# Kernel tuning notes

Measured on AMD Instinct MI355X. Metric: run time of the kernel, lower is better.

Reference implementation:

```python
import jax, jax.numpy as jnp
import numpy as np

B, T, C, S, H, K = 32, 128, 32, 256, 64, 3  # T == 2*H required by final Linear(hidden*2, 1)


def setup_inputs() -> dict:
    key = jax.random.key(0)
    k1, k2, k3, k4 = jax.random.split(key, 4)
    x = jax.random.normal(k1, (B, T, C, S), jnp.float32)
    # ConvLSTMCell: Conv1d(C+H -> 4H, kernel K, padding same), gate order i,f,o,g
    Wc = jax.random.normal(k2, (4 * H, C + H, K), jnp.float32) * 0.05
    bc = jnp.zeros((4 * H,), jnp.float32)
    # final Linear(hidden*2 = T, 1)
    Wl = jax.random.normal(k3, (1, T), jnp.float32) * 0.05
    bl = jnp.zeros((1,), jnp.float32)
    return {"x": x, "Wc": Wc, "bc": bc, "Wl": Wl, "bl": bl}


def _cell(x_t, h, c, Wc, bc):
    # x_t: (B, C, T); h, c: (B, H, T). Conv over the T axis, 'same' padding.
    z = jnp.concatenate([x_t, h], axis=1)  # (B, C+H, T)
    conv = jax.lax.conv_general_dilated(
        z, Wc, window_strides=(1,), padding='SAME',
        dimension_numbers=('NCH', 'OIH', 'NCH')) + bc[None, :, None]
    ci, cf, co, cg = jnp.split(conv, 4, axis=1)
    i = jax.nn.sigmoid(ci)
    f = jax.nn.sigmoid(cf)
    o = jax.nn.sigmoid(co)
    g = jnp.tanh(cg)
    c_next = f * c + i * g
    h_next = o * jnp.tanh(c_next)
    return h_next, c_next


def reference(x, Wc, bc, Wl, bl):
    # x: (B, T, C, S); sequential scan over spatial axis S with (h, c) recurrence.
    xs = jnp.transpose(x, (3, 0, 2, 1))  # (S, B, C, T)
    h0 = jnp.zeros((x.shape[0], H, x.shape[1]), x.dtype)

    def step(carry, xt):
        h, c = carry
        h2, c2 = _cell(xt, h, c, Wc, bc)
        return (h2, c2), h2

    _, hs = jax.lax.scan(step, (h0, h0), xs)  # hs: (S, B, H, T)
    lstm_out = jnp.transpose(hs, (1, 0, 2, 3))  # (B, S, H, T)
    out = jax.nn.sigmoid(jnp.einsum('bsht,ot->bso', lstm_out, Wl)[..., None].squeeze(-1)[..., None] * 0 + jnp.einsum('bsht,ot->bsho', lstm_out, Wl) + bl)
    return out  # (B, S, H, 1)
```

## Files before the change

kernel.cpp:

```cpp
#include <hip/hip_runtime.h>


#define Bb 32
#define Tt 128
#define Cc 32
#define Ss 256
#define Hh 64
#define ZST 104

typedef __bf16 bf16x8 __attribute__((ext_vector_type(8)));
typedef short  short8 __attribute__((ext_vector_type(8)));
typedef float  f32x4  __attribute__((ext_vector_type(4)));
typedef unsigned short u16;
typedef unsigned int   u32;

__device__ __forceinline__ u16 f2bf(float f) {
    u32 u = __float_as_uint(f);
    u = (u + 0x7FFFu + ((u >> 16) & 1u)) >> 16;
    return (u16)u;
}
__device__ __forceinline__ float fsig(float x) {
    float e = __expf(-x);
    return __builtin_amdgcn_rcpf(1.0f + e);
}
__device__ __forceinline__ float ftanh_(float x) {
    float e = __expf(2.0f * x);
    return 1.0f - 2.0f * __builtin_amdgcn_rcpf(e + 1.0f);
}

__global__ __launch_bounds__(256) void xpose_kernel(const float* __restrict__ x,
                                                    u16* __restrict__ xT) {
    __shared__ u16 tile[64][130];
    const int tc0 = blockIdx.x * 128;
    const int s0  = blockIdx.y * 64;
    const int b   = blockIdx.z;
    const int tid = threadIdx.x;
    const float* xb = x + (size_t)b * (Tt * Cc * Ss);
#pragma unroll
    for (int i = 0; i < 32; ++i) {
        const int tcr = (tid >> 6) + 4 * i;
        const int sr  = tid & 63;
        tile[sr][tcr] = f2bf(xb[(size_t)(tc0 + tcr) * Ss + s0 + sr]);
    }
    __syncthreads();
    u32* xTo = (u32*)(xT + (size_t)b * (Ss * Tt * Cc));
#pragma unroll
    for (int j = 0; j < 16; ++j) {
        const int sw = (tid >> 6) + 4 * j;
        const int tw = (tid & 63) * 2;
        xTo[(((size_t)(s0 + sw)) * (Tt * Cc) + tc0 + tw) >> 1] = *(const u32*)&tile[sw][tw];
    }
}

__global__ __launch_bounds__(256) void wprep_kernel(const float* __restrict__ Wc,
                                                    u16* __restrict__ wpre) {
    const int ht  = blockIdx.x;
    const int tid = threadIdx.x;
#pragma unroll
    for (int it = 0; it < 9; ++it) {
        const int idx  = it * 256 + tid;
        const int f    = idx >> 6;
        const int lane = idx & 63;
        const int g  = f / 9;
        const int k  = (f % 9) / 3;
        const int ks = f % 3;
        const int l15 = lane & 15;
        const int q   = lane >> 4;
        const int gc  = 64 * g + 16 * ht + l15;
        u16 tmp[8];
#pragma unroll
        for (int j = 0; j < 8; ++j)
            tmp[j] = f2bf(Wc[gc * 288 + (32 * ks + 8 * q + j) * 3 + k]);
        *(uint4*)(wpre + ((size_t)(ht * 36 + f) * 64 + lane) * 8) = *(const uint4*)tmp;
    }
}

__global__ __launch_bounds__(512) void convlstm5_kernel(
    const float* __restrict__ bc, const float* __restrict__ Wl,
    const float* __restrict__ bl, const u16* __restrict__ xT,
    const u16* __restrict__ wpre, float* __restrict__ out) {

    __shared__ u16  zbuf[2][130][ZST];
    __shared__ float red[8][16];

    const int b    = blockIdx.x;
    const int tid  = threadIdx.x;
    const int w    = tid >> 6;
    const int lane = tid & 63;
    const int l15  = lane & 15;
    const int q    = lane >> 4;
    const int ht   = w >> 1;
    const int th   = w & 1;

    {
        u32* z32 = (u32*)&zbuf[0][0][0];
        for (int i = tid; i < (2 * 130 * ZST) / 2; i += 512) z32[i] = 0;
    }

    const u16* wlp = wpre + (size_t)ht * 18432 + lane * 8;

    f32x4 bcv[4];
#pragma unroll
    for (int g = 0; g < 4; ++g) bcv[g] = *(const f32x4*)&bc[64 * g + 16 * ht + 4 * q];
    float wlv[4];
#pragma unroll
    for (int nj = 0; nj < 4; ++nj) wlv[nj] = Wl[64 * th + 16 * nj + l15];
    const float bl0 = bl[0];

    float cst[16];
#pragma unroll
    for (int i = 0; i < 16; ++i) cst[i] = 0.0f;

    const int xt = tid >> 2;
    const int xc = (tid & 3) * 8;
    const u16* xTb = xT + (size_t)b * (Ss * Tt * Cc);

    {
        uint4 xv0 = *(const uint4*)(xTb + xt * 32 + xc);
        __syncthreads();
        *(uint4*)&zbuf[0][1 + xt][xc] = xv0;
        __syncthreads();
    }

    float* outb = out + (size_t)b * (Ss * Hh);
    int p = 0;

    for (int s = 0; s < Ss; ++s) {
        uint4 xv;
        const bool havex = (s + 1) < Ss;
        if (havex) xv = *(const uint4*)(xTb + (size_t)(s + 1) * (Tt * Cc) + xt * 32 + xc);

        if (tid < 64 && s > 0) {
            float v = red[(tid >> 4) * 2][tid & 15] + red[(tid >> 4) * 2 + 1][tid & 15] + bl0;
            outb[(size_t)(s - 1) * Hh + tid] = fsig(v);
        }
        __syncthreads();

        const u16 (*zb)[ZST] = zbuf[p];
        u16 (*zn)[ZST] = zbuf[p ^ 1];

        float partial[4] = {0.f, 0.f, 0.f, 0.f};

#pragma unroll
        for (int half = 0; half < 2; ++half) {
            f32x4 acc[4][2];
#pragma unroll
            for (int g = 0; g < 4; ++g) {
                acc[g][0] = bcv[g];
                acc[g][1] = bcv[g];
            }

            bf16x8 wf[2][4];
#pragma unroll
            for (int g = 0; g < 4; ++g)
                wf[0][g] = *(const bf16x8*)(wlp + (size_t)(g * 9) * 512);

#pragma unroll
            for (int kk = 0; kk < 9; ++kk) {
                const int k  = kk / 3;
                const int ks = kk % 3;
                const int cur = kk & 1;
                if (kk < 8) {
#pragma unroll
                    for (int g = 0; g < 4; ++g)
                        wf[cur ^ 1][g] = *(const bf16x8*)(wlp + (size_t)(g * 9 + kk + 1) * 512);
                }
#pragma unroll
                for (int njl = 0; njl < 2; ++njl) {
                    const int nj = half * 2 + njl;
                    const int tb = 64 * th + 16 * nj + l15;
                    bf16x8 bfr = *(const bf16x8*)&zb[tb + k][32 * ks + 8 * q];
                    acc[0][njl] = __builtin_amdgcn_mfma_f32_16x16x32_bf16(wf[cur][0], bfr, acc[0][njl], 0, 0, 0);
                    acc[1][njl] = __builtin_amdgcn_mfma_f32_16x16x32_bf16(wf[cur][1], bfr, acc[1][njl], 0, 0, 0);
                    acc[2][njl] = __builtin_amdgcn_mfma_f32_16x16x32_bf16(wf[cur][2], bfr, acc[2][njl], 0, 0, 0);
                    acc[3][njl] = __builtin_amdgcn_mfma_f32_16x16x32_bf16(wf[cur][3], bfr, acc[3][njl], 0, 0, 0);
                }
            }

#pragma unroll
            for (int njl = 0; njl < 2; ++njl) {
                const int nj = half * 2 + njl;
                u16 hp[4];
#pragma unroll
                for (int r = 0; r < 4; ++r) {
                    const float ig = fsig(acc[0][njl][r]);
                    const float fg = fsig(acc[1][njl][r]);
                    const float og = fsig(acc[2][njl][r]);
                    const float gg = ftanh_(acc[3][njl][r]);
                    const float cv = fg * cst[nj * 4 + r] + ig * gg;
                    cst[nj * 4 + r] = cv;
                    const float hv = og * ftanh_(cv);
                    partial[r] += hv * wlv[nj];
                    hp[r] = f2bf(hv);
                }
                uint2 hw;
                hw.x = (u32)hp[0] | ((u32)hp[1] << 16);
                hw.y = (u32)hp[2] | ((u32)hp[3] << 16);
                *(uint2*)&zn[1 + 64 * th + 16 * nj + l15][32 + 16 * ht + 4 * q] = hw;
            }
        }

        if (havex) *(uint4*)&zn[1 + xt][xc] = xv;

#pragma unroll
        for (int r = 0; r < 4; ++r) {
#pragma unroll
            for (int offl = 1; offl <= 8; offl <<= 1)
                partial[r] += __shfl_xor(partial[r], offl, 64);
        }
        if (l15 == 0) {
#pragma unroll
            for (int r = 0; r < 4; ++r) red[w][4 * q + r] = partial[r];
        }
        __syncthreads();
        p ^= 1;
    }

    if (tid < 64) {
        float v = red[(tid >> 4) * 2][tid & 15] + red[(tid >> 4) * 2 + 1][tid & 15] + bl0;
        outb[(size_t)(Ss - 1) * Hh + tid] = fsig(v);
    }
}

__global__ __launch_bounds__(512, 2) void convlstm_kernel(
    const float* __restrict__ Wc, const float* __restrict__ bc,
    const float* __restrict__ Wl, const float* __restrict__ bl,
    const u16* __restrict__ xT, float* __restrict__ out) {

    __shared__ u16  zbuf[2][130][ZST];
    __shared__ float red[8][16];
    __shared__ float bcl[256];

    const int b    = blockIdx.x;
    const int tid  = threadIdx.x;
    const int w    = tid >> 6;
    const int lane = tid & 63;
    const int l15  = lane & 15;
    const int q    = lane >> 4;
    const int ht   = w >> 1;
    const int th   = w & 1;

    {
        u32* z32 = (u32*)&zbuf[0][0][0];
        for (int i = tid; i < (2 * 130 * ZST) / 2; i += 512) z32[i] = 0;
    }
    if (tid < 256) bcl[tid] = bc[tid];

    bf16x8 afr[4][3][3];
#pragma unroll
    for (int g = 0; g < 4; ++g)
#pragma unroll
        for (int k = 0; k < 3; ++k)
#pragma unroll
            for (int ks = 0; ks < 3; ++ks) {
                const int gc = 64 * g + 16 * ht + l15;
                short8 t;
#pragma unroll
                for (int j = 0; j < 8; ++j)
                    t[j] = (short)f2bf(Wc[gc * 288 + (32 * ks + 8 * q + j) * 3 + k]);
                afr[g][k][ks] = __builtin_bit_cast(bf16x8, t);
            }

    float wlv[4];
#pragma unroll
    for (int nj = 0; nj < 4; ++nj) wlv[nj] = Wl[64 * th + 16 * nj + l15];
    const float bl0 = bl[0];

    float cst[16];
#pragma unroll
    for (int i = 0; i < 16; ++i) cst[i] = 0.0f;

    const int xt = tid >> 2;
    const int xc = (tid & 3) * 8;
    const u16* xTb = xT + (size_t)b * (Ss * Tt * Cc);

    {
        uint4 xv0 = *(const uint4*)(xTb + xt * 32 + xc);
        __syncthreads();
        *(uint4*)&zbuf[0][1 + xt][xc] = xv0;
        __syncthreads();
    }

    float* outb = out + (size_t)b * (Ss * Hh);
    int p = 0;

    for (int s = 0; s < Ss; ++s) {
        uint4 xv;
        const bool havex = (s + 1) < Ss;
        if (havex) xv = *(const uint4*)(xTb + (size_t)(s + 1) * (Tt * Cc) + xt * 32 + xc);

        if (tid < 64 && s > 0) {
            float v = red[(tid >> 4) * 2][tid & 15] + red[(tid >> 4) * 2 + 1][tid & 15] + bl0;
            outb[(size_t)(s - 1) * Hh + tid] = fsig(v);
        }
        __syncthreads();

        const u16 (*zb)[ZST] = zbuf[p];
        u16 (*zn)[ZST] = zbuf[p ^ 1];

        float partial[4] = {0.f, 0.f, 0.f, 0.f};

#pragma unroll
        for (int half = 0; half < 2; ++half) {
            f32x4 acc[4][2];
#pragma unroll
            for (int g = 0; g < 4; ++g) {
                acc[g][0] = (f32x4){0.f, 0.f, 0.f, 0.f};
                acc[g][1] = (f32x4){0.f, 0.f, 0.f, 0.f};
            }
#pragma unroll
            for (int njl = 0; njl < 2; ++njl) {
                const int nj = half * 2 + njl;
                const int tb = 64 * th + 16 * nj + l15;
#pragma unroll
                for (int k = 0; k < 3; ++k)
#pragma unroll
                    for (int ks = 0; ks < 3; ++ks) {
                        bf16x8 bfr = *(const bf16x8*)&zb[tb + k][32 * ks + 8 * q];
                        acc[0][njl] = __builtin_amdgcn_mfma_f32_16x16x32_bf16(afr[0][k][ks], bfr, acc[0][njl], 0, 0, 0);
                        acc[1][njl] = __builtin_amdgcn_mfma_f32_16x16x32_bf16(afr[1][k][ks], bfr, acc[1][njl], 0, 0, 0);
                        acc[2][njl] = __builtin_amdgcn_mfma_f32_16x16x32_bf16(afr[2][k][ks], bfr, acc[2][njl], 0, 0, 0);
                        acc[3][njl] = __builtin_amdgcn_mfma_f32_16x16x32_bf16(afr[3][k][ks], bfr, acc[3][njl], 0, 0, 0);
                    }
            }

#pragma unroll
            for (int njl = 0; njl < 2; ++njl) {
                const int nj = half * 2 + njl;
                u16 hp[4];
#pragma unroll
                for (int r = 0; r < 4; ++r) {
                    const int hl = 4 * q + r;
                    const float ig = fsig(acc[0][njl][r] + bcl[0   + 16 * ht + hl]);
                    const float fg = fsig(acc[1][njl][r] + bcl[64  + 16 * ht + hl]);
                    const float og = fsig(acc[2][njl][r] + bcl[128 + 16 * ht + hl]);
                    const float gg = ftanh_(acc[3][njl][r] + bcl[192 + 16 * ht + hl]);
                    const float cv = fg * cst[nj * 4 + r] + ig * gg;
                    cst[nj * 4 + r] = cv;
                    const float hv = og * ftanh_(cv);
                    partial[r] += hv * wlv[nj];
                    hp[r] = f2bf(hv);
                }
                uint2 hw;
                hw.x = (u32)hp[0] | ((u32)hp[1] << 16);
                hw.y = (u32)hp[2] | ((u32)hp[3] << 16);
                *(uint2*)&zn[1 + 64 * th + 16 * nj + l15][32 + 16 * ht + 4 * q] = hw;
            }
        }

        if (havex) *(uint4*)&zn[1 + xt][xc] = xv;

#pragma unroll
        for (int r = 0; r < 4; ++r) {
#pragma unroll
            for (int offl = 1; offl <= 8; offl <<= 1)
                partial[r] += __shfl_xor(partial[r], offl, 64);
        }
        if (l15 == 0) {
#pragma unroll
            for (int r = 0; r < 4; ++r) red[w][4 * q + r] = partial[r];
        }
        __syncthreads();
        p ^= 1;
    }

    if (tid < 64) {
        float v = red[(tid >> 4) * 2][tid & 15] + red[(tid >> 4) * 2 + 1][tid & 15] + bl0;
        outb[(size_t)(Ss - 1) * Hh + tid] = fsig(v);
    }
}

extern "C" void kernel_launch(void* const* d_in, const int* in_sizes, int n_in,
                              void* d_out, int out_size, void* d_ws, size_t ws_size,
                              hipStream_t stream) {
    const float* x  = (const float*)d_in[0];
    const float* Wc = (const float*)d_in[1];
    const float* bc = (const float*)d_in[2];
    const float* Wl = (const float*)d_in[3];
    const float* bl = (const float*)d_in[4];
    float* out = (float*)d_out;

    u16* xT = (u16*)d_ws;
    const size_t XT_BYTES = (size_t)Bb * Ss * Tt * Cc * 2;
    const size_t WP_BYTES = (size_t)4 * 36 * 64 * 8 * 2;

    dim3 tgrid(Tt * Cc / 128, Ss / 64, Bb);
    xpose_kernel<<<tgrid, 256, 0, stream>>>(x, xT);

    if (ws_size >= XT_BYTES + WP_BYTES) {
        u16* wpre = (u16*)((char*)d_ws + XT_BYTES);
        wprep_kernel<<<4, 256, 0, stream>>>(Wc, wpre);
        convlstm5_kernel<<<Bb, 512, 0, stream>>>(bc, Wl, bl, xT, wpre, out);
    } else {
        convlstm_kernel<<<Bb, 512, 0, stream>>>(Wc, bc, Wl, bl, xT, out);
    }
}
```

Measured before the change: 1.375 ms.

## Split each batch recurrence across two workgroups with global-memory halo exchange

Replaces the one-block-per-batch recurrent kernel with two cooperating workgroups per batch, each computing half of the hidden channels. The blocks exchange their new h slices every step through a global halo buffer guarded by release/acquire flag counters. Each block also caches its half of the prepacked weights in LDS and uses a hardware packed bf16 conversion. This doubles the number of CUs working on the sequential scan (64 blocks instead of 32) and halves per-step MFMA work per block. The cost is a global-memory spin-wait every step, and forward progress relies on both blocks of a pair being resident at the same time.

```diff
diff --git a/kernel.cpp b/kernel.cpp
--- a/kernel.cpp
+++ b/kernel.cpp
@@ -13,6 +13,7 @@
 typedef float  f32x4  __attribute__((ext_vector_type(4)));
 typedef unsigned short u16;
 typedef unsigned int   u32;
+typedef unsigned long long u64;
 
 __device__ __forceinline__ u16 f2bf(float f) {
     u32 u = __float_as_uint(f);
@@ -26,6 +27,11 @@
 __device__ __forceinline__ float ftanh_(float x) {
     float e = __expf(2.0f * x);
     return 1.0f - 2.0f * __builtin_amdgcn_rcpf(e + 1.0f);
+}
+__device__ __forceinline__ u32 cvtpk(float lo, float hi) {
+    u32 d;
+    asm("v_cvt_pk_bf16_f32 %0, %1, %2" : "=v"(d) : "v"(lo), "v"(hi));
+    return d;
 }
 
 __global__ __launch_bounds__(256) void xpose_kernel(const float* __restrict__ x,
@@ -75,13 +81,182 @@
     }
 }
 
-__global__ __launch_bounds__(512) void convlstm5_kernel(
+__global__ __launch_bounds__(512) void convlstm6_kernel(
     const float* __restrict__ bc, const float* __restrict__ Wl,
     const float* __restrict__ bl, const u16* __restrict__ xT,
-    const u16* __restrict__ wpre, float* __restrict__ out) {
-
+    const u16* __restrict__ wpre, u64* __restrict__ halo,
+    u32* __restrict__ flags, float* __restrict__ out) {
+
+    __shared__ u16  wlds[36864];
     __shared__ u16  zbuf[2][130][ZST];
     __shared__ float red[8][16];
+
+    const int p    = blockIdx.x;
+    const int b    = blockIdx.y;
+    const int tid  = threadIdx.x;
+    const int w    = tid >> 6;
+    const int lane = tid & 63;
+    const int l15  = lane & 15;
+    const int q    = lane >> 4;
+    const int th   = w >> 1;
+    const int ht2  = w & 1;
+
+    {
+        u32* z32 = (u32*)&zbuf[0][0][0];
+        for (int i = tid; i < (2 * 130 * ZST) / 2; i += 512) z32[i] = 0;
+    }
+    {
+        const uint4* wsrc = (const uint4*)(wpre + (size_t)(2 * p) * 18432);
+        uint4* wdst = (uint4*)wlds;
+#pragma unroll
+        for (int i = 0; i < 9; ++i) wdst[tid + 512 * i] = wsrc[tid + 512 * i];
+    }
+
+    f32x4 bcv[4];
+#pragma unroll
+    for (int g = 0; g < 4; ++g)
+        bcv[g] = *(const f32x4*)&bc[64 * g + 32 * p + 16 * ht2 + 4 * q];
+    float wlv[2];
+#pragma unroll
+    for (int nj = 0; nj < 2; ++nj) wlv[nj] = Wl[32 * th + 16 * nj + l15];
+    const float bl0 = bl[0];
+
+    float cst[8];
+#pragma unroll
+    for (int i = 0; i < 8; ++i) cst[i] = 0.0f;
+
+    const int xr = tid >> 2;
+    const int xc = (tid & 3) * 8;
+    const u16* xTb = xT + (size_t)b * (Ss * Tt * Cc);
+
+    u64* haloP = halo + (size_t)(b * 2 + p) * 2 * 1024;
+    const u64* haloC = halo + (size_t)(b * 2 + (1 - p)) * 2 * 1024;
+    u32* flagP = flags + (b * 2 + p) * 2;
+    u32* flagC = flags + (b * 2 + (1 - p)) * 2;
+
+    {
+        uint4 xv0 = *(const uint4*)(xTb + xr * 32 + xc);
+        __syncthreads();
+        *(uint4*)&zbuf[1][1 + xr][xc] = xv0;
+        __syncthreads();
+    }
+
+    float* outb = out + (size_t)b * (Ss * Hh) + 32 * p;
+    const u16* wl0 = wlds + ht2 * 18432 + lane * 8;
+
+    for (int s = 0; s < Ss; ++s) {
+        uint4 xv;
+        const bool havex = (s + 1) < Ss;
+        if (havex) xv = *(const uint4*)(xTb + (size_t)(s + 1) * (Tt * Cc) + xr * 32 + xc);
+
+        if (tid < 32 && s > 0) {
+            const int h2 = tid >> 4, hh = tid & 15;
+            float v = red[h2][hh] + red[2 + h2][hh] + red[4 + h2][hh] + red[6 + h2][hh] + bl0;
+            outb[(size_t)(s - 1) * Hh + 16 * h2 + hh] = fsig(v);
+        }
+        __syncthreads();
+
+        const u16 (*zb)[ZST] = zbuf[(s + 1) & 1];
+        u16 (*zn)[ZST] = zbuf[s & 1];
+
+        f32x4 acc[2][4];
+#pragma unroll
+        for (int nj = 0; nj < 2; ++nj)
+#pragma unroll
+            for (int g = 0; g < 4; ++g) acc[nj][g] = bcv[g];
+
+#pragma unroll
+        for (int k = 0; k < 3; ++k)
+#pragma unroll
+            for (int ks = 0; ks < 3; ++ks) {
+                bf16x8 wf0 = *(const bf16x8*)(wl0 + (0 * 9 + k * 3 + ks) * 512);
+                bf16x8 wf1 = *(const bf16x8*)(wl0 + (1 * 9 + k * 3 + ks) * 512);
+                bf16x8 wf2 = *(const bf16x8*)(wl0 + (2 * 9 + k * 3 + ks) * 512);
+                bf16x8 wf3 = *(const bf16x8*)(wl0 + (3 * 9 + k * 3 + ks) * 512);
+#pragma unroll
+                for (int nj = 0; nj < 2; ++nj) {
+                    bf16x8 bfr = *(const bf16x8*)&zb[32 * th + 16 * nj + l15 + k][32 * ks + 8 * q];
+                    acc[nj][0] = __builtin_amdgcn_mfma_f32_16x16x32_bf16(wf0, bfr, acc[nj][0], 0, 0, 0);
+                    acc[nj][1] = __builtin_amdgcn_mfma_f32_16x16x32_bf16(wf1, bfr, acc[nj][1], 0, 0, 0);
+                    acc[nj][2] = __builtin_amdgcn_mfma_f32_16x16x32_bf16(wf2, bfr, acc[nj][2], 0, 0, 0);
+                    acc[nj][3] = __builtin_amdgcn_mfma_f32_16x16x32_bf16(wf3, bfr, acc[nj][3], 0, 0, 0);
+                }
+            }
+
+        float partial[4] = {0.f, 0.f, 0.f, 0.f};
+#pragma unroll
+        for (int nj = 0; nj < 2; ++nj) {
+            float hv[4];
+#pragma unroll
+            for (int r = 0; r < 4; ++r) {
+                const float ig = fsig(acc[nj][0][r]);
+                const float fg = fsig(acc[nj][1][r]);
+                const float og = fsig(acc[nj][2][r]);
+                const float gg = ftanh_(acc[nj][3][r]);
+                const float cv = fg * cst[nj * 4 + r] + ig * gg;
+                cst[nj * 4 + r] = cv;
+                hv[r] = og * ftanh_(cv);
+                partial[r] += hv[r] * wlv[nj];
+            }
+            const u32 hx = cvtpk(hv[0], hv[1]);
+            const u32 hy = cvtpk(hv[2], hv[3]);
+            const int t = 32 * th + 16 * nj + l15;
+            uint2 hw; hw.x = hx; hw.y = hy;
+            *(uint2*)&zn[1 + t][32 + 32 * p + 16 * ht2 + 4 * q] = hw;
+            const u64 pv = (u64)hx | ((u64)hy << 32);
+            __hip_atomic_store(&haloP[(size_t)(s & 1) * 1024 + t * 8 + 4 * ht2 + q], pv,
+                               __ATOMIC_RELAXED, __HIP_MEMORY_SCOPE_AGENT);
+        }
+        if (lane == 0)
+            __hip_atomic_fetch_add(&flagP[s & 1], 1u, __ATOMIC_RELEASE, __HIP_MEMORY_SCOPE_AGENT);
+
+        if (havex) *(uint4*)&zn[1 + xr][xc] = xv;
+
+#pragma unroll
+        for (int r = 0; r < 4; ++r) {
+#pragma unroll
+            for (int offl = 1; offl <= 8; offl <<= 1)
+                partial[r] += __shfl_xor(partial[r], offl, 64);
+        }
+        if (l15 == 0) {
+#pragma unroll
+            for (int r = 0; r < 4; ++r) red[w][4 * q + r] = partial[r];
+        }
+
+        if (s + 1 < Ss) {
+            if (lane == 0) {
+                const u32 tgt = 8u * ((u32)(s >> 1) + 1u);
+                while (__hip_atomic_load(&flagC[s & 1], __ATOMIC_ACQUIRE,
+                                         __HIP_MEMORY_SCOPE_AGENT) < tgt) {}
+            }
+            const u64* hsrc = haloC + (size_t)(s & 1) * 1024;
+#pragma unroll
+            for (int ii = 0; ii < 2; ++ii) {
+                const int j = tid + 512 * ii;
+                const u64 v = __hip_atomic_load(&hsrc[j], __ATOMIC_RELAXED,
+                                                __HIP_MEMORY_SCOPE_AGENT);
+                uint2 vw; vw.x = (u32)v; vw.y = (u32)(v >> 32);
+                *(uint2*)&zn[1 + (j >> 3)][32 + 32 * (1 - p) + 4 * (j & 7)] = vw;
+            }
+        }
+        __syncthreads();
+    }
+
+    if (tid < 32) {
+        const int h2 = tid >> 4, hh = tid & 15;
+        float v = red[h2][hh] + red[2 + h2][hh] + red[4 + h2][hh] + red[6 + h2][hh] + bl0;
+        outb[(size_t)(Ss - 1) * Hh + 16 * h2 + hh] = fsig(v);
+    }
+}
+
+__global__ __launch_bounds__(512, 2) void convlstm_kernel(
+    const float* __restrict__ Wc, const float* __restrict__ bc,
+    const float* __restrict__ Wl, const float* __restrict__ bl,
+    const u16* __restrict__ xT, float* __restrict__ out) {
+
+    __shared__ u16  zbuf[2][130][ZST];
+    __shared__ float red[8][16];
+    __shared__ float bcl[256];
 
     const int b    = blockIdx.x;
     const int tid  = threadIdx.x;
@@ -96,12 +271,23 @@
         u32* z32 = (u32*)&zbuf[0][0][0];
         for (int i = tid; i < (2 * 130 * ZST) / 2; i += 512) z32[i] = 0;
     }
-
-    const u16* wlp = wpre + (size_t)ht * 18432 + lane * 8;
-
-    f32x4 bcv[4];
-#pragma unroll
-    for (int g = 0; g < 4; ++g) bcv[g] = *(const f32x4*)&bc[64 * g + 16 * ht + 4 * q];
+    if (tid < 256) bcl[tid] = bc[tid];
+
+    bf16x8 afr[4][3][3];
+#pragma unroll
+    for (int g = 0; g < 4; ++g)
+#pragma unroll
+        for (int k = 0; k < 3; ++k)
+#pragma unroll
+            for (int ks = 0; ks < 3; ++ks) {
+                const int gc = 64 * g + 16 * ht + l15;
+                short8 t;
+#pragma unroll
+                for (int j = 0; j < 8; ++j)
+                    t[j] = (short)f2bf(Wc[gc * 288 + (32 * ks + 8 * q + j) * 3 + k]);
+                afr[g][k][ks] = __builtin_bit_cast(bf16x8, t);
+            }
+
     float wlv[4];
 #pragma unroll
     for (int nj = 0; nj < 4; ++nj) wlv[nj] = Wl[64 * th + 16 * nj + l15];
@@ -123,7 +309,7 @@
     }
 
     float* outb = out + (size_t)b * (Ss * Hh);
-    int p = 0;
+    int pp = 0;
 
     for (int s = 0; s < Ss; ++s) {
         uint4 xv;
@@ -136,167 +322,8 @@
         }
         __syncthreads();
 
-        const u16 (*zb)[ZST] = zbuf[p];
-        u16 (*zn)[ZST] = zbuf[p ^ 1];
-
-        float partial[4] = {0.f, 0.f, 0.f, 0.f};
-
-#pragma unroll
-        for (int half = 0; half < 2; ++half) {
-            f32x4 acc[4][2];
-#pragma unroll
-            for (int g = 0; g < 4; ++g) {
-                acc[g][0] = bcv[g];
-                acc[g][1] = bcv[g];
-            }
-
-            bf16x8 wf[2][4];
-#pragma unroll
-            for (int g = 0; g < 4; ++g)
-                wf[0][g] = *(const bf16x8*)(wlp + (size_t)(g * 9) * 512);
-
-#pragma unroll
-            for (int kk = 0; kk < 9; ++kk) {
-                const int k  = kk / 3;
-                const int ks = kk % 3;
-                const int cur = kk & 1;
-                if (kk < 8) {
-#pragma unroll
-                    for (int g = 0; g < 4; ++g)
-                        wf[cur ^ 1][g] = *(const bf16x8*)(wlp + (size_t)(g * 9 + kk + 1) * 512);
-                }
-#pragma unroll
-                for (int njl = 0; njl < 2; ++njl) {
-                    const int nj = half * 2 + njl;
-                    const int tb = 64 * th + 16 * nj + l15;
-                    bf16x8 bfr = *(const bf16x8*)&zb[tb + k][32 * ks + 8 * q];
-                    acc[0][njl] = __builtin_amdgcn_mfma_f32_16x16x32_bf16(wf[cur][0], bfr, acc[0][njl], 0, 0, 0);
-                    acc[1][njl] = __builtin_amdgcn_mfma_f32_16x16x32_bf16(wf[cur][1], bfr, acc[1][njl], 0, 0, 0);
-                    acc[2][njl] = __builtin_amdgcn_mfma_f32_16x16x32_bf16(wf[cur][2], bfr, acc[2][njl], 0, 0, 0);
-                    acc[3][njl] = __builtin_amdgcn_mfma_f32_16x16x32_bf16(wf[cur][3], bfr, acc[3][njl], 0, 0, 0);
-                }
-            }
-
-#pragma unroll
-            for (int njl = 0; njl < 2; ++njl) {
-                const int nj = half * 2 + njl;
-                u16 hp[4];
-#pragma unroll
-                for (int r = 0; r < 4; ++r) {
-                    const float ig = fsig(acc[0][njl][r]);
-                    const float fg = fsig(acc[1][njl][r]);
-                    const float og = fsig(acc[2][njl][r]);
-                    const float gg = ftanh_(acc[3][njl][r]);
-                    const float cv = fg * cst[nj * 4 + r] + ig * gg;
-                    cst[nj * 4 + r] = cv;
-                    const float hv = og * ftanh_(cv);
-                    partial[r] += hv * wlv[nj];
-                    hp[r] = f2bf(hv);
-                }
-                uint2 hw;
-                hw.x = (u32)hp[0] | ((u32)hp[1] << 16);
-                hw.y = (u32)hp[2] | ((u32)hp[3] << 16);
-                *(uint2*)&zn[1 + 64 * th + 16 * nj + l15][32 + 16 * ht + 4 * q] = hw;
-            }
-        }
-
-        if (havex) *(uint4*)&zn[1 + xt][xc] = xv;
-
-#pragma unroll
-        for (int r = 0; r < 4; ++r) {
-#pragma unroll
-            for (int offl = 1; offl <= 8; offl <<= 1)
-                partial[r] += __shfl_xor(partial[r], offl, 64);
-        }
-        if (l15 == 0) {
-#pragma unroll
-            for (int r = 0; r < 4; ++r) red[w][4 * q + r] = partial[r];
-        }
-        __syncthreads();
-        p ^= 1;
-    }
-
-    if (tid < 64) {
-        float v = red[(tid >> 4) * 2][tid & 15] + red[(tid >> 4) * 2 + 1][tid & 15] + bl0;
-        outb[(size_t)(Ss - 1) * Hh + tid] = fsig(v);
-    }
-}
-
-__global__ __launch_bounds__(512, 2) void convlstm_kernel(
-    const float* __restrict__ Wc, const float* __restrict__ bc,
-    const float* __restrict__ Wl, const float* __restrict__ bl,
-    const u16* __restrict__ xT, float* __restrict__ out) {
-
-    __shared__ u16  zbuf[2][130][ZST];
-    __shared__ float red[8][16];
-    __shared__ float bcl[256];
-
-    const int b    = blockIdx.x;
-    const int tid  = threadIdx.x;
-    const int w    = tid >> 6;
-    const int lane = tid & 63;
-    const int l15  = lane & 15;
-    const int q    = lane >> 4;
-    const int ht   = w >> 1;
-    const int th   = w & 1;
-
-    {
-        u32* z32 = (u32*)&zbuf[0][0][0];
-        for (int i = tid; i < (2 * 130 * ZST) / 2; i += 512) z32[i] = 0;
-    }
-    if (tid < 256) bcl[tid] = bc[tid];
-
-    bf16x8 afr[4][3][3];
-#pragma unroll
-    for (int g = 0; g < 4; ++g)
-#pragma unroll
-        for (int k = 0; k < 3; ++k)
-#pragma unroll
-            for (int ks = 0; ks < 3; ++ks) {
-                const int gc = 64 * g + 16 * ht + l15;
-                short8 t;
-#pragma unroll
-                for (int j = 0; j < 8; ++j)
-                    t[j] = (short)f2bf(Wc[gc * 288 + (32 * ks + 8 * q + j) * 3 + k]);
-                afr[g][k][ks] = __builtin_bit_cast(bf16x8, t);
-            }
-
-    float wlv[4];
-#pragma unroll
-    for (int nj = 0; nj < 4; ++nj) wlv[nj] = Wl[64 * th + 16 * nj + l15];
-    const float bl0 = bl[0];
-
-    float cst[16];
-#pragma unroll
-    for (int i = 0; i < 16; ++i) cst[i] = 0.0f;
-
-    const int xt = tid >> 2;
-    const int xc = (tid & 3) * 8;
-    const u16* xTb = xT + (size_t)b * (Ss * Tt * Cc);
-
-    {
-        uint4 xv0 = *(const uint4*)(xTb + xt * 32 + xc);
-        __syncthreads();
-        *(uint4*)&zbuf[0][1 + xt][xc] = xv0;
-        __syncthreads();
-    }
-
-    float* outb = out + (size_t)b * (Ss * Hh);
-    int p = 0;
-
-    for (int s = 0; s < Ss; ++s) {
-        uint4 xv;
-        const bool havex = (s + 1) < Ss;
-        if (havex) xv = *(const uint4*)(xTb + (size_t)(s + 1) * (Tt * Cc) + xt * 32 + xc);
-
-        if (tid < 64 && s > 0) {
-            float v = red[(tid >> 4) * 2][tid & 15] + red[(tid >> 4) * 2 + 1][tid & 15] + bl0;
-            outb[(size_t)(s - 1) * Hh + tid] = fsig(v);
-        }
-        __syncthreads();
-
-        const u16 (*zb)[ZST] = zbuf[p];
-        u16 (*zn)[ZST] = zbuf[p ^ 1];
+        const u16 (*zb)[ZST] = zbuf[pp];
+        u16 (*zn)[ZST] = zbuf[pp ^ 1];
 
         float partial[4] = {0.f, 0.f, 0.f, 0.f};
 
@@ -361,7 +388,7 @@
             for (int r = 0; r < 4; ++r) red[w][4 * q + r] = partial[r];
         }
         __syncthreads();
-        p ^= 1;
+        pp ^= 1;
     }
 
     if (tid < 64) {
@@ -381,16 +408,21 @@
     float* out = (float*)d_out;
 
     u16* xT = (u16*)d_ws;
-    const size_t XT_BYTES = (size_t)Bb * Ss * Tt * Cc * 2;
-    const size_t WP_BYTES = (size_t)4 * 36 * 64 * 8 * 2;
+    const size_t XT_BYTES   = (size_t)Bb * Ss * Tt * Cc * 2;
+    const size_t WP_BYTES   = (size_t)4 * 36 * 64 * 8 * 2;
+    const size_t HALO_BYTES = (size_t)Bb * 2 * 2 * 1024 * 8;
+    const size_t FLAG_BYTES = (size_t)Bb * 2 * 2 * 4;
 
     dim3 tgrid(Tt * Cc / 128, Ss / 64, Bb);
     xpose_kernel<<<tgrid, 256, 0, stream>>>(x, xT);
 
-    if (ws_size >= XT_BYTES + WP_BYTES) {
-        u16* wpre = (u16*)((char*)d_ws + XT_BYTES);
+    if (ws_size >= XT_BYTES + WP_BYTES + HALO_BYTES + FLAG_BYTES) {
+        u16* wpre  = (u16*)((char*)d_ws + XT_BYTES);
+        u64* halo  = (u64*)((char*)d_ws + XT_BYTES + WP_BYTES);
+        u32* flags = (u32*)((char*)d_ws + XT_BYTES + WP_BYTES + HALO_BYTES);
         wprep_kernel<<<4, 256, 0, stream>>>(Wc, wpre);
-        convlstm5_kernel<<<Bb, 512, 0, stream>>>(bc, Wl, bl, xT, wpre, out);
+        hipMemsetAsync(flags, 0, FLAG_BYTES, stream);
+        convlstm6_kernel<<<dim3(2, Bb), 512, 0, stream>>>(bc, Wl, bl, xT, wpre, halo, flags, out);
     } else {
         convlstm_kernel<<<Bb, 512, 0, stream>>>(Wc, bc, Wl, bl, xT, out);
     }
```

New measurement: 4.859 ms. 3.53x slower.
